# Optimization experiments

Measured on AMD Instinct MI355X. Metric: run time of the kernel, lower is better.

Reference implementation:

```python
import jax, jax.numpy as jnp
import numpy as np


def _grid_sample_points(feat, gx, gy):
    """Bilinear grid_sample at point list, align_corners=False, zeros padding.
    feat: [B, H, W, C]; gx, gy: [B, N] normalized coords in [-1, 1].
    Returns [B, N, C].
    """
    B, H, W, C = feat.shape
    # unnormalize (align_corners=False): -1 -> -0.5, +1 -> size-0.5
    ix = (gx + 1.0) * (W * 0.5) - 0.5
    iy = (gy + 1.0) * (H * 0.5) - 0.5
    x0 = jnp.floor(ix)
    y0 = jnp.floor(iy)
    x1 = x0 + 1.0
    y1 = y0 + 1.0
    wx1 = ix - x0
    wx0 = 1.0 - wx1
    wy1 = iy - y0
    wy0 = 1.0 - wy1
    bidx = jnp.arange(B)[:, None]  # [B,1] broadcasts against [B,N]

    def gather(yy, xx):
        valid = (xx >= 0) & (xx <= W - 1) & (yy >= 0) & (yy <= H - 1)
        xi = jnp.clip(xx, 0, W - 1).astype(jnp.int32)
        yi = jnp.clip(yy, 0, H - 1).astype(jnp.int32)
        v = feat[bidx, yi, xi]  # [B, N, C]
        return v * valid[..., None].astype(feat.dtype)

    out = (gather(y0, x0) * (wy0 * wx0)[..., None]
           + gather(y0, x1) * (wy0 * wx1)[..., None]
           + gather(y1, x0) * (wy1 * wx0)[..., None]
           + gather(y1, x1) * (wy1 * wx1)[..., None])
    return out


def setup_inputs() -> dict:
    key = jax.random.key(0)
    k1, k2, k3, k4, k5 = jax.random.split(key, 5)
    B, C, T, Wd, Hd = 16, 64, 16, 36, 36
    N, D = 4096, C * T  # num_neurons, num_input
    x = jax.random.normal(k1, (B, C, T, Wd, Hd), dtype=jnp.float32)
    mu = jax.random.uniform(k2, (N, 2), minval=-1.0, maxval=1.0, dtype=jnp.float32)
    sigma = jax.random.uniform(k3, (N,), dtype=jnp.float32)  # unused in eval mode
    W = jax.random.normal(k4, (N, D), dtype=jnp.float32) * 0.02
    b = jax.random.normal(k5, (N,), dtype=jnp.float32) * 0.01
    return {"x": x, "mu": mu, "sigma": sigma, "W": W, "b": b}


def reference(x, mu, sigma, W, b):
    # eval-mode forward (self.training == False): grid = mu broadcast over batch
    B, C, T, Wd, Hd = x.shape
    N = mu.shape[0]
    # torch: x.view(B, C*T, Wd, Hd); grid_sample treats dim2 as H_in, dim3 as W_in
    feat = x.reshape(B, C * T, Wd, Hd).transpose(0, 2, 3, 1)
    g = jnp.clip(mu, -1.0, 1.0)
    gx = jnp.broadcast_to(g[:, 0], (B, N))  # grid[...,0] indexes W_in
    gy = jnp.broadcast_to(g[:, 1], (B, N))  # grid[...,1] indexes H_in
    sampled = _grid_sample_points(feat, gx, gy)  # [B, N, C*T]
    # PoissonLinearReadout 3D path == per-neuron dot product (diagonal of full matmul)
    y = jnp.einsum('bnc,nc->bn', sampled, W) + b
    return jax.nn.elu(y) + 1.0
```

## Files before the change

### kernel.cpp

```cpp
#include <hip/hip_runtime.h>
#include <hip/hip_bf16.h>
#include <cmath>

#define CT    1024
#define PIX   1296
#define BATCH 16
#define NNEUR 4096
#define HW    36
#define NBINS (HW * HW)
#define NB    4
#define BQ    4
#define BCT   (BATCH * CT)

#define SORT_BLK   1
#define PACK_BLKS  2048
#define TRAN_BLKS  (41 * 16 * 16)
#define STAGE_GRID (SORT_BLK + PACK_BLKS + TRAN_BLKS)

#if defined(__has_builtin)
#  if __has_builtin(__builtin_amdgcn_fdot2_f32_bf16)
#    define HAVE_FDOT2_BF16 1
#  endif
#endif
#ifndef HAVE_FDOT2_BF16
#  define HAVE_FDOT2_BF16 0
#endif

typedef __bf16 bf16x2 __attribute__((ext_vector_type(2)));
__device__ __forceinline__ bf16x2 as_bf16x2(unsigned u) {
    union { unsigned u; bf16x2 v; } cv; cv.u = u; return cv.v;
}
__device__ __forceinline__ unsigned short bfu(float f) {
    __hip_bfloat16 h = __float2bfloat16(f);
    return *reinterpret_cast<unsigned short*>(&h);
}
__device__ __forceinline__ float bflo(unsigned u) { return __uint_as_float(u << 16); }
__device__ __forceinline__ float bfhi(unsigned u) { return __uint_as_float(u & 0xFFFF0000u); }

__global__ __launch_bounds__(256) void stage_kernel(
    const float* __restrict__ x, __hip_bfloat16* __restrict__ feat,
    const float* __restrict__ mu, int* __restrict__ perm,
    const float* __restrict__ W, __hip_bfloat16* __restrict__ Wb)
{
    const int bid = blockIdx.x;
    const int t   = threadIdx.x;

    __shared__ int hist[NBINS];
    __shared__ int chunkSum[48];
    __shared__ unsigned short lds[64][34];

    if (bid == 0) {
        for (int i = t; i < NBINS; i += 256) hist[i] = 0;
        __syncthreads();
        int key[16];
#pragma unroll
        for (int j = 0; j < 16; ++j) {
            const int n = t * 16 + j;
            float gx = fminf(fmaxf(mu[2 * n],     -1.f), 1.f);
            float gy = fminf(fmaxf(mu[2 * n + 1], -1.f), 1.f);
            float ix = (gx + 1.f) * (HW * 0.5f) - 0.5f;
            float iy = (gy + 1.f) * (HW * 0.5f) - 0.5f;
            int xi = min(max((int)floorf(ix), 0), HW - 1);
            int yi = min(max((int)floorf(iy), 0), HW - 1);
            key[j] = yi * HW + xi;
            atomicAdd(&hist[key[j]], 1);
        }
        __syncthreads();
        if (t < 41) {
            int s = 0;
            for (int i = 0; i < 32; ++i) {
                int idx = t * 32 + i;
                if (idx < NBINS) s += hist[idx];
            }
            chunkSum[t] = s;
        }
        __syncthreads();
        if (t == 0) {
            int run = 0;
            for (int i = 0; i < 41; ++i) { int v = chunkSum[i]; chunkSum[i] = run; run += v; }
        }
        __syncthreads();
        if (t < 41) {
            int run = chunkSum[t];
            for (int i = 0; i < 32; ++i) {
                int idx = t * 32 + i;
                if (idx < NBINS) { int v = hist[idx]; hist[idx] = run; run += v; }
            }
        }
        __syncthreads();
#pragma unroll
        for (int j = 0; j < 16; ++j) {
            const int n = t * 16 + j;
            const int pos = atomicAdd(&hist[key[j]], 1);
            perm[pos] = n;
        }
        return;
    }

    if (bid <= PACK_BLKS) {
        const size_t i = ((size_t)(bid - 1) * 256 + t) * 2;
        const float4 a = reinterpret_cast<const float4*>(W)[i];
        const float4 b = reinterpret_cast<const float4*>(W)[i + 1];
        unsigned short o[8] = { bfu(a.x), bfu(a.y), bfu(a.z), bfu(a.w),
                                bfu(b.x), bfu(b.y), bfu(b.z), bfu(b.w) };
        reinterpret_cast<uint4*>((unsigned short*)Wb)[((size_t)(bid - 1) * 256 + t)] =
            *reinterpret_cast<uint4*>(o);
        return;
    }

    const int flat   = bid - 1 - PACK_BLKS;
    const int pBase  = (flat % 41) * 32;
    const int ctBase = ((flat / 41) % 16) * 64;
    const int b      = flat / (41 * 16);
    const size_t xb  = (size_t)b * CT * PIX;
    {
        const int r  = t >> 2;
        const int pc = (t & 3) * 8;
        const float* src = x + xb + (size_t)(ctBase + r) * PIX + pBase + pc;
        if (pBase + 32 <= PIX) {
            float4 a = reinterpret_cast<const float4*>(src)[0];
            float4 c = reinterpret_cast<const float4*>(src)[1];
            lds[r][pc + 0] = bfu(a.x); lds[r][pc + 1] = bfu(a.y);
            lds[r][pc + 2] = bfu(a.z); lds[r][pc + 3] = bfu(a.w);
            lds[r][pc + 4] = bfu(c.x); lds[r][pc + 5] = bfu(c.y);
            lds[r][pc + 6] = bfu(c.z); lds[r][pc + 7] = bfu(c.w);
        } else {
#pragma unroll
            for (int i = 0; i < 8; ++i) {
                int p = pBase + pc + i;
                lds[r][pc + i] = (p < PIX) ? bfu(src[i]) : (unsigned short)0;
            }
        }
    }
    __syncthreads();
    const int pr = t >> 3;
    const int cc = (t & 7) * 8;
    if (pBase + pr < PIX) {
        unsigned short o[8];
#pragma unroll
        for (int i = 0; i < 8; ++i) o[i] = lds[cc + i][pr];
        const size_t off = ((size_t)(pBase + pr) * BATCH + b) * CT + ctBase + cc;
        *reinterpret_cast<uint4*>((unsigned short*)feat + off) = *reinterpret_cast<uint4*>(o);
    }
}

__global__ __launch_bounds__(256, 4) void readout_bf16_kernel(
    const __hip_bfloat16* __restrict__ feat,
    const float* __restrict__ mu,
    const __hip_bfloat16* __restrict__ Wb,
    const float* __restrict__ bias,
    const int* __restrict__ perm,
    float* __restrict__ out)
{
    const int bid = blockIdx.x;
    const int xcd = bid & 7;
    const int r   = bid >> 3;
    const int g   = xcd * 128 + (r >> 2);
    const int q   = r & 3;
    const int t = threadIdx.x;
    const int c = t & 127;
    const int h = t >> 7;

    const int4 nids = *reinterpret_cast<const int4*>(perm + g * NB);
    const int nid[NB] = { nids.x, nids.y, nids.z, nids.w };

    uint4 wq[NB];
#pragma unroll
    for (int nb = 0; nb < NB; ++nb)
        wq[nb] = reinterpret_cast<const uint4*>(Wb + (size_t)nid[nb] * CT)[c];

#if !HAVE_FDOT2_BF16
    float w[NB][8];
#pragma unroll
    for (int nb = 0; nb < NB; ++nb) {
        w[nb][0] = bflo(wq[nb].x); w[nb][1] = bfhi(wq[nb].x);
        w[nb][2] = bflo(wq[nb].y); w[nb][3] = bfhi(wq[nb].y);
        w[nb][4] = bflo(wq[nb].z); w[nb][5] = bfhi(wq[nb].z);
        w[nb][6] = bflo(wq[nb].w); w[nb][7] = bfhi(wq[nb].w);
    }
#endif

    __shared__ float wmat16[16][NB];
    __shared__ int   upix[16];
    __shared__ float uw[16][NB];
    __shared__ int   ucount_s;

    if (t < 16) {
#pragma unroll
        for (int j = 0; j < NB; ++j) wmat16[t][j] = 0.f;
    }

    int   mypix = -1;
    float mycw  = 0.f;
    if (t < 16) {
        const int nb = t >> 2, k = t & 3;
        const int n = nid[nb];
        float gx = fminf(fmaxf(mu[2 * n],     -1.f), 1.f);
        float gy = fminf(fmaxf(mu[2 * n + 1], -1.f), 1.f);
        float ix = (gx + 1.f) * (HW * 0.5f) - 0.5f;
        float iy = (gy + 1.f) * (HW * 0.5f) - 0.5f;
        float x0f = floorf(ix), y0f = floorf(iy);
        float wx1 = ix - x0f, wx0 = 1.f - wx1;
        float wy1 = iy - y0f, wy0 = 1.f - wy1;
        int xx = (int)x0f + (k & 1), yy = (int)y0f + (k >> 1);
        bool valid = (xx >= 0) && (xx < HW) && (yy >= 0) && (yy < HW);
        int xi = min(max(xx, 0), HW - 1), yi = min(max(yy, 0), HW - 1);
        mypix = yi * HW + xi;
        mycw  = ((k & 1) ? wx1 : wx0) * ((k >> 1) ? wy1 : wy0) * (valid ? 1.f : 0.f);
    }

    int myslot = 15;
#pragma unroll
    for (int j = 15; j >= 0; --j) {
        int pj = __shfl(mypix, j, 64);
        if (pj == mypix) myslot = j;
    }
    if (t < 16) atomicAdd(&wmat16[myslot][t >> 2], mycw);

    const bool uniq = (t < 16) && (myslot == t);
    const unsigned long long mask = __ballot(uniq);
    if (t == 0) ucount_s = __popcll(mask);
    const int pix0 = __shfl(mypix, 0, 64);
    __syncthreads();

    const int U    = ucount_s;
    const int Upad = (U + 7) & ~7;
    if (uniq) {
        const int pos = __popcll(mask & ((1ull << t) - 1));
        upix[pos] = mypix;
#pragma unroll
        for (int j = 0; j < NB; ++j) uw[pos][j] = wmat16[t][j];
    }
    if (t >= U && t < Upad) {
        upix[t] = pix0;
#pragma unroll
        for (int j = 0; j < NB; ++j) uw[t][j] = 0.f;
    }
    __syncthreads();

    float acc[NB][2];
#pragma unroll
    for (int nb = 0; nb < NB; ++nb) { acc[nb][0] = 0.f; acc[nb][1] = 0.f; }

    const int b0 = q * BQ + h * 2;
    const unsigned short* fb = (const unsigned short*)feat + (size_t)b0 * CT + (size_t)c * 8;

    for (int u = 0; u < Upad; u += 8) {
        int poff[8];
#pragma unroll
        for (int s = 0; s < 8; ++s) poff[s] = upix[u + s] * BCT;
        uint4 va[8], vb[8];
#pragma unroll
        for (int s = 0; s < 8; ++s) {
            va[s] = *reinterpret_cast<const uint4*>(fb + poff[s]);
            vb[s] = *reinterpret_cast<const uint4*>(fb + poff[s] + CT);
        }
#pragma unroll
        for (int s = 0; s < 8; ++s) {
            const float4 pw = *reinterpret_cast<const float4*>(uw[u + s]);
            const float pws[NB] = { pw.x, pw.y, pw.z, pw.w };
#if HAVE_FDOT2_BF16
#pragma unroll
            for (int nb = 0; nb < NB; ++nb) {
                if (pws[nb] != 0.f) {
                    float d0 = __builtin_amdgcn_fdot2_f32_bf16(as_bf16x2(va[s].x), as_bf16x2(wq[nb].x), 0.f, false);
                    float d1 = __builtin_amdgcn_fdot2_f32_bf16(as_bf16x2(vb[s].x), as_bf16x2(wq[nb].x), 0.f, false);
                    d0 = __builtin_amdgcn_fdot2_f32_bf16(as_bf16x2(va[s].y), as_bf16x2(wq[nb].y), d0, false);
                    d1 = __builtin_amdgcn_fdot2_f32_bf16(as_bf16x2(vb[s].y), as_bf16x2(wq[nb].y), d1, false);
                    d0 = __builtin_amdgcn_fdot2_f32_bf16(as_bf16x2(va[s].z), as_bf16x2(wq[nb].z), d0, false);
                    d1 = __builtin_amdgcn_fdot2_f32_bf16(as_bf16x2(vb[s].z), as_bf16x2(wq[nb].z), d1, false);
                    d0 = __builtin_amdgcn_fdot2_f32_bf16(as_bf16x2(va[s].w), as_bf16x2(wq[nb].w), d0, false);
                    d1 = __builtin_amdgcn_fdot2_f32_bf16(as_bf16x2(vb[s].w), as_bf16x2(wq[nb].w), d1, false);
                    acc[nb][0] = fmaf(pws[nb], d0, acc[nb][0]);
                    acc[nb][1] = fmaf(pws[nb], d1, acc[nb][1]);
                }
            }
#else
            float fa[8] = { bflo(va[s].x), bfhi(va[s].x), bflo(va[s].y), bfhi(va[s].y),
                            bflo(va[s].z), bfhi(va[s].z), bflo(va[s].w), bfhi(va[s].w) };
            float fbv[8] = { bflo(vb[s].x), bfhi(vb[s].x), bflo(vb[s].y), bfhi(vb[s].y),
                             bflo(vb[s].z), bfhi(vb[s].z), bflo(vb[s].w), bfhi(vb[s].w) };
#pragma unroll
            for (int nb = 0; nb < NB; ++nb) {
                if (pws[nb] != 0.f) {
                    float d0 = fa[0]  * w[nb][0];
                    float d1 = fbv[0] * w[nb][0];
#pragma unroll
                    for (int j = 1; j < 8; ++j) {
                        d0 = fmaf(fa[j],  w[nb][j], d0);
                        d1 = fmaf(fbv[j], w[nb][j], d1);
                    }
                    acc[nb][0] = fmaf(pws[nb], d0, acc[nb][0]);
                    acc[nb][1] = fmaf(pws[nb], d1, acc[nb][1]);
                }
            }
#endif
        }
    }

    __shared__ float red[4][NB][2];
#pragma unroll
    for (int nb = 0; nb < NB; ++nb) {
#pragma unroll
        for (int i = 0; i < 2; ++i) {
            float v = acc[nb][i];
#pragma unroll
            for (int off = 32; off > 0; off >>= 1)
                v += __shfl_down(v, off, 64);
            acc[nb][i] = v;
        }
    }
    const int wave = t >> 6, lane = t & 63;
    if (lane == 0) {
#pragma unroll
        for (int nb = 0; nb < NB; ++nb) {
            red[wave][nb][0] = acc[nb][0];
            red[wave][nb][1] = acc[nb][1];
        }
    }
    __syncthreads();
    if (t < NB * BQ) {
        const int nb = t >> 2, bl = t & 3;
        const int hh = bl >> 1, i = bl & 1;
        float y = red[hh * 2][nb][i] + red[hh * 2 + 1][nb][i] + bias[nid[nb]];
        const int b = q * BQ + bl;
        out[(size_t)b * NNEUR + nid[nb]] = (y > 0.f) ? (y + 1.f) : expf(y);
    }
}

__global__ __launch_bounds__(256) void readout_f32_strided_kernel(
    const float* __restrict__ x,
    const float* __restrict__ mu,
    const float* __restrict__ Wm,
    const float* __restrict__ bias,
    float* __restrict__ out)
{
    const int n = blockIdx.x;
    const int t = threadIdx.x;
    const float4 w4 = reinterpret_cast<const float4*>(Wm + (size_t)n * CT)[t];
    float gx = fminf(fmaxf(mu[2 * n],     -1.f), 1.f);
    float gy = fminf(fmaxf(mu[2 * n + 1], -1.f), 1.f);
    float ix = (gx + 1.f) * (HW * 0.5f) - 0.5f;
    float iy = (gy + 1.f) * (HW * 0.5f) - 0.5f;
    float x0f = floorf(ix), y0f = floorf(iy);
    float wx1 = ix - x0f, wx0 = 1.f - wx1;
    float wy1 = iy - y0f, wy0 = 1.f - wy1;
    int x0 = (int)x0f, y0 = (int)y0f;
    float cw[4]; int cp[4];
#pragma unroll
    for (int k = 0; k < 4; ++k) {
        int xx = x0 + (k & 1), yy = y0 + (k >> 1);
        bool valid = (xx >= 0) && (xx < HW) && (yy >= 0) && (yy < HW);
        int xi = min(max(xx, 0), HW - 1), yi = min(max(yy, 0), HW - 1);
        cp[k] = yi * HW + xi;
        cw[k] = ((k & 1) ? wx1 : wx0) * ((k >> 1) ? wy1 : wy0) * (valid ? 1.f : 0.f);
    }
    float acc[BATCH];
#pragma unroll
    for (int b = 0; b < BATCH; ++b) {
        float s = 0.f;
#pragma unroll
        for (int k = 0; k < 4; ++k) {
            if (cw[k] != 0.f) {
                const float* fp = x + (size_t)b * CT * PIX + cp[k];
                const int c0 = 4 * t;
                s += cw[k] * (fp[(size_t)(c0 + 0) * PIX] * w4.x
                            + fp[(size_t)(c0 + 1) * PIX] * w4.y
                            + fp[(size_t)(c0 + 2) * PIX] * w4.z
                            + fp[(size_t)(c0 + 3) * PIX] * w4.w);
            }
        }
        acc[b] = s;
    }
#pragma unroll
    for (int b = 0; b < BATCH; ++b) {
        float v = acc[b];
#pragma unroll
        for (int off = 32; off > 0; off >>= 1)
            v += __shfl_down(v, off, 64);
        acc[b] = v;
    }
    __shared__ float red[4][BATCH];
    const int wave = t >> 6, lane = t & 63;
    if (lane == 0) {
#pragma unroll
        for (int b = 0; b < BATCH; ++b) red[wave][b] = acc[b];
    }
    __syncthreads();
    if (t < BATCH) {
        float y = red[0][t] + red[1][t] + red[2][t] + red[3][t] + bias[n];
        out[(size_t)t * NNEUR + n] = (y > 0.f) ? (y + 1.f) : expf(y);
    }
}

extern "C" void kernel_launch(void* const* d_in, const int* in_sizes, int n_in,
                              void* d_out, int out_size, void* d_ws, size_t ws_size,
                              hipStream_t stream)
{
    const float* x    = (const float*)d_in[0];
    const float* mu   = (const float*)d_in[1];
    const float* Wm   = (const float*)d_in[3];
    const float* bias = (const float*)d_in[4];
    float* out = (float*)d_out;

    const size_t featBytes = (size_t)BATCH * PIX * CT * sizeof(__hip_bfloat16);
    const size_t wBytes    = (size_t)NNEUR * CT * sizeof(__hip_bfloat16);
    const size_t permBytes = (size_t)NNEUR * sizeof(int);
    if (ws_size >= featBytes + wBytes + permBytes) {
        __hip_bfloat16* feat = (__hip_bfloat16*)d_ws;
        __hip_bfloat16* Wb   = (__hip_bfloat16*)((char*)d_ws + featBytes);
        int* perm = (int*)((char*)d_ws + featBytes + wBytes);
        stage_kernel<<<STAGE_GRID, 256, 0, stream>>>(x, feat, mu, perm, Wm, Wb);
        readout_bf16_kernel<<<(NNEUR / NB) * (BATCH / BQ), 256, 0, stream>>>(
            feat, mu, Wb, bias, perm, out);
    } else {
        readout_f32_strided_kernel<<<NNEUR, 256, 0, stream>>>(x, mu, Wm, bias, out);
    }
}
```

Before: 57.28 us.

## Process eight neurons per readout block to share sampled pixel loads

Raises the number of neurons per block from four to eight, so each block gathers up to 32 bilinear taps, deduplicates them, and reuses each loaded feature pixel across more neurons' dot products. It halves the number of blocks, drops the minimum-occupancy launch bound, and replaces the padded-pixel loop with a masked tail that clamps indices. The extra weight registers and accumulators raise register pressure and may lower occupancy. Whether more shared pixels are found depends on how the sort groups spatially nearby neurons.

Measured after the change: 59.08 us. +3.1%, slower.

```diff
diff --git a/kernel.cpp b/kernel.cpp
--- a/kernel.cpp
+++ b/kernel.cpp
@@ -8,7 +8,7 @@
 #define NNEUR 4096
 #define HW    36
 #define NBINS (HW * HW)
-#define NB    4
+#define NB    8
 #define BQ    4
 #define BCT   (BATCH * CT)
 
@@ -144,7 +144,7 @@
     }
 }
 
-__global__ __launch_bounds__(256, 4) void readout_bf16_kernel(
+__global__ __launch_bounds__(256) void readout_bf16_kernel(
     const __hip_bfloat16* __restrict__ feat,
     const float* __restrict__ mu,
     const __hip_bfloat16* __restrict__ Wb,
@@ -155,44 +155,34 @@
     const int bid = blockIdx.x;
     const int xcd = bid & 7;
     const int r   = bid >> 3;
-    const int g   = xcd * 128 + (r >> 2);
+    const int g   = xcd * 64 + (r >> 2);
     const int q   = r & 3;
     const int t = threadIdx.x;
     const int c = t & 127;
     const int h = t >> 7;
 
-    const int4 nids = *reinterpret_cast<const int4*>(perm + g * NB);
-    const int nid[NB] = { nids.x, nids.y, nids.z, nids.w };
+    const int4 nA = *reinterpret_cast<const int4*>(perm + g * NB);
+    const int4 nB = *reinterpret_cast<const int4*>(perm + g * NB + 4);
+    const int nid[NB] = { nA.x, nA.y, nA.z, nA.w, nB.x, nB.y, nB.z, nB.w };
 
     uint4 wq[NB];
 #pragma unroll
     for (int nb = 0; nb < NB; ++nb)
         wq[nb] = reinterpret_cast<const uint4*>(Wb + (size_t)nid[nb] * CT)[c];
 
-#if !HAVE_FDOT2_BF16
-    float w[NB][8];
-#pragma unroll
-    for (int nb = 0; nb < NB; ++nb) {
-        w[nb][0] = bflo(wq[nb].x); w[nb][1] = bfhi(wq[nb].x);
-        w[nb][2] = bflo(wq[nb].y); w[nb][3] = bfhi(wq[nb].y);
-        w[nb][4] = bflo(wq[nb].z); w[nb][5] = bfhi(wq[nb].z);
-        w[nb][6] = bflo(wq[nb].w); w[nb][7] = bfhi(wq[nb].w);
-    }
-#endif
-
-    __shared__ float wmat16[16][NB];
-    __shared__ int   upix[16];
-    __shared__ float uw[16][NB];
+    __shared__ float wmat[32][NB];
+    __shared__ int   upix[32];
+    __shared__ float uw[32][NB];
     __shared__ int   ucount_s;
 
-    if (t < 16) {
-#pragma unroll
-        for (int j = 0; j < NB; ++j) wmat16[t][j] = 0.f;
+    if (t < 32) {
+#pragma unroll
+        for (int j = 0; j < NB; ++j) wmat[t][j] = 0.f;
     }
 
     int   mypix = -1;
     float mycw  = 0.f;
-    if (t < 16) {
+    if (t < 32) {
         const int nb = t >> 2, k = t & 3;
         const int n = nid[nb];
         float gx = fminf(fmaxf(mu[2 * n],     -1.f), 1.f);
@@ -209,32 +199,25 @@
         mycw  = ((k & 1) ? wx1 : wx0) * ((k >> 1) ? wy1 : wy0) * (valid ? 1.f : 0.f);
     }
 
-    int myslot = 15;
-#pragma unroll
-    for (int j = 15; j >= 0; --j) {
+    int myslot = 63;
+#pragma unroll
+    for (int j = 31; j >= 0; --j) {
         int pj = __shfl(mypix, j, 64);
         if (pj == mypix) myslot = j;
     }
-    if (t < 16) atomicAdd(&wmat16[myslot][t >> 2], mycw);
-
-    const bool uniq = (t < 16) && (myslot == t);
+    if (t < 32) atomicAdd(&wmat[myslot][t >> 2], mycw);
+
+    const bool uniq = (t < 32) && (myslot == t);
     const unsigned long long mask = __ballot(uniq);
     if (t == 0) ucount_s = __popcll(mask);
-    const int pix0 = __shfl(mypix, 0, 64);
     __syncthreads();
 
-    const int U    = ucount_s;
-    const int Upad = (U + 7) & ~7;
+    const int U = ucount_s;
     if (uniq) {
         const int pos = __popcll(mask & ((1ull << t) - 1));
         upix[pos] = mypix;
 #pragma unroll
-        for (int j = 0; j < NB; ++j) uw[pos][j] = wmat16[t][j];
-    }
-    if (t >= U && t < Upad) {
-        upix[t] = pix0;
-#pragma unroll
-        for (int j = 0; j < NB; ++j) uw[t][j] = 0.f;
+        for (int j = 0; j < NB; ++j) uw[pos][j] = wmat[t][j];
     }
     __syncthreads();
 
@@ -245,10 +228,17 @@
     const int b0 = q * BQ + h * 2;
     const unsigned short* fb = (const unsigned short*)feat + (size_t)b0 * CT + (size_t)c * 8;
 
-    for (int u = 0; u < Upad; u += 8) {
-        int poff[8];
-#pragma unroll
-        for (int s = 0; s < 8; ++s) poff[s] = upix[u + s] * BCT;
+    for (int u = 0; u < U; u += 8) {
+        int   uidx[8];
+        float umsk[8];
+        int   poff[8];
+#pragma unroll
+        for (int s = 0; s < 8; ++s) {
+            const int idx = u + s;
+            umsk[s] = (idx < U) ? 1.f : 0.f;
+            uidx[s] = min(idx, U - 1);
+            poff[s] = upix[uidx[s]] * BCT;
+        }
         uint4 va[8], vb[8];
 #pragma unroll
         for (int s = 0; s < 8; ++s) {
@@ -257,8 +247,12 @@
         }
 #pragma unroll
         for (int s = 0; s < 8; ++s) {
-            const float4 pw = *reinterpret_cast<const float4*>(uw[u + s]);
-            const float pws[NB] = { pw.x, pw.y, pw.z, pw.w };
+            const float4 pw0 = *reinterpret_cast<const float4*>(&uw[uidx[s]][0]);
+            const float4 pw1 = *reinterpret_cast<const float4*>(&uw[uidx[s]][4]);
+            const float pws[NB] = { pw0.x * umsk[s], pw0.y * umsk[s],
+                                    pw0.z * umsk[s], pw0.w * umsk[s],
+                                    pw1.x * umsk[s], pw1.y * umsk[s],
+                                    pw1.z * umsk[s], pw1.w * umsk[s] };
 #if HAVE_FDOT2_BF16
 #pragma unroll
             for (int nb = 0; nb < NB; ++nb) {
@@ -283,13 +277,18 @@
 #pragma unroll
             for (int nb = 0; nb < NB; ++nb) {
                 if (pws[nb] != 0.f) {
-                    float d0 = fa[0]  * w[nb][0];
-                    float d1 = fbv[0] * w[nb][0];
-#pragma unroll
-                    for (int j = 1; j < 8; ++j) {
-                        d0 = fmaf(fa[j],  w[nb][j], d0);
-                        d1 = fmaf(fbv[j], w[nb][j], d1);
-                    }
+                    float w0 = bflo(wq[nb].x), w1 = bfhi(wq[nb].x);
+                    float w2 = bflo(wq[nb].y), w3 = bfhi(wq[nb].y);
+                    float w4 = bflo(wq[nb].z), w5 = bfhi(wq[nb].z);
+                    float w6 = bflo(wq[nb].w), w7 = bfhi(wq[nb].w);
+                    float d0 = fa[0] * w0, d1 = fbv[0] * w0;
+                    d0 = fmaf(fa[1], w1, d0); d1 = fmaf(fbv[1], w1, d1);
+                    d0 = fmaf(fa[2], w2, d0); d1 = fmaf(fbv[2], w2, d1);
+                    d0 = fmaf(fa[3], w3, d0); d1 = fmaf(fbv[3], w3, d1);
+                    d0 = fmaf(fa[4], w4, d0); d1 = fmaf(fbv[4], w4, d1);
+                    d0 = fmaf(fa[5], w5, d0); d1 = fmaf(fbv[5], w5, d1);
+                    d0 = fmaf(fa[6], w6, d0); d1 = fmaf(fbv[6], w6, d1);
+                    d0 = fmaf(fa[7], w7, d0); d1 = fmaf(fbv[7], w7, d1);
                     acc[nb][0] = fmaf(pws[nb], d0, acc[nb][0]);
                     acc[nb][1] = fmaf(pws[nb], d1, acc[nb][1]);
                 }
```
